# Kernel optimization log

Measured on AMD Instinct MI355X. Metric: run time of the kernel, lower is better.

## Reference

```python
import jax, jax.numpy as jnp
from jax import lax
import numpy as np

B, T, F = 64, 128, 16
H = 512
S = 2  # num_seg; SEG_DICT['2'] = [8, 6], seg_cumsum = [2, 10, 16]


def timestep_embedding(t, dim, max_period=10000.0):
    half = dim // 2
    freqs = jnp.exp(-jnp.log(max_period) * jnp.arange(half, dtype=jnp.float32) / half)
    args = t[:, None] * freqs  # [N, half]
    return jnp.concatenate([jnp.cos(args), jnp.sin(args)], axis=-1)  # [N, dim]


def setup_inputs() -> dict:
    key = jax.random.key(0)
    ks = jax.random.split(key, 16)
    sc = lambda *sh: 1.0 / np.sqrt(sh[-1])
    inp = {
        'x': jax.random.normal(ks[0], (B, T, F), dtype=jnp.float32),
        'lengths': jax.random.randint(ks[1], (B,), 1, T + 1),
        'h0': jax.random.uniform(ks[2], (B, H), dtype=jnp.float32),
        'c0': jax.random.uniform(ks[3], (B, H), dtype=jnp.float32),
        'W_is0': jax.random.normal(ks[4], (H, 8), dtype=jnp.float32) * sc(8),
        'b_is0': jax.random.normal(ks[5], (H,), dtype=jnp.float32) * 0.01,
        'W_is1': jax.random.normal(ks[6], (H, 6), dtype=jnp.float32) * sc(6),
        'b_is1': jax.random.normal(ks[7], (H,), dtype=jnp.float32) * 0.01,
        'W_ih': jax.random.normal(ks[8], (4 * H, 3 * H), dtype=jnp.float32) * sc(3 * H),
        'W_hh': jax.random.normal(ks[9], (4 * H, H), dtype=jnp.float32) * sc(H),
        'b_ih': jax.random.normal(ks[10], (4 * H,), dtype=jnp.float32) * 0.01,
        'b_hh': jax.random.normal(ks[11], (4 * H,), dtype=jnp.float32) * 0.01,
        'W_o': jax.random.normal(ks[12], (F - 2, S * H), dtype=jnp.float32) * sc(S * H),
        'b_o': jax.random.normal(ks[13], (F - 2,), dtype=jnp.float32) * 0.01,
    }
    return inp


def reference(x, lengths, h0, c0, W_is0, b_is0, W_is1, b_is1,
              W_ih, W_hh, b_ih, b_hh, W_o, b_o):
    b, t, f = x.shape
    h = h0.shape[1]
    xf = x.reshape(-1, f)  # [B*T, F]

    # timestep embeddings from the two time columns (learning_type='diff')
    tc = timestep_embedding(xf[:, 0], h)
    tp = timestep_embedding(xf[:, 1], h)
    t_emb = jnp.concatenate([tc, tp], axis=-1)  # [B*T, 2H]

    # per-segment input linears (segments = cols 2:10 and 10:16)
    e0 = xf[:, 2:10] @ W_is0.T + b_is0
    e1 = xf[:, 10:16] @ W_is1.T + b_is1
    e0 = jnp.concatenate([e0, t_emb], axis=-1)[:, None, :]  # [B*T, 1, 3H]
    e1 = jnp.concatenate([e1, t_emb], axis=-1)[:, None, :]
    # faithful to torch: concat on dim=1 then reshape(batch, num_seg, seq_len, -1)
    embs = jnp.concatenate([e0, e1], axis=1).reshape(b, S, t, 3 * h)

    def cell(carry, xt):
        hh, cc = carry
        gates = xt @ W_ih.T + b_ih + hh @ W_hh.T + b_hh
        i, fg, g, o = jnp.split(gates, 4, axis=-1)  # torch LSTMCell order i,f,g,o
        cc = jax.nn.sigmoid(fg) * cc + jax.nn.sigmoid(i) * jnp.tanh(g)
        hh = jax.nn.sigmoid(o) * jnp.tanh(cc)
        return (hh, cc), hh

    hs = []
    for s in range(S):  # shared cell weights across segments (same nn.LSTMCell object)
        xs = jnp.swapaxes(embs[:, s], 0, 1)  # [T, B, 3H]
        _, h_seq = lax.scan(cell, (h0, c0), xs)  # [T, B, H]
        hs.append(jnp.swapaxes(h_seq, 0, 1))  # [B, T, H]
    hidden_states = jnp.stack(hs, axis=-2)  # [B, T, S, H]; dropout rate 0 -> identity

    idx = lengths - 1  # final valid timestep per sequence
    hfin = hidden_states[jnp.arange(b), idx].reshape(b, S * h)  # [B, S*H]
    out = jax.nn.sigmoid(hfin @ W_o.T + b_o)  # mlp_o: Linear + Sigmoid
    return out
```

## Files before the change

kernel.cpp:

```cpp
#include <hip/hip_runtime.h>
#include <hip/hip_bf16.h>
#include <stdint.h>


typedef __attribute__((ext_vector_type(8))) short bf16x8_t;
typedef __attribute__((ext_vector_type(4))) float f32x4_t;

#define SENT 0xAAAAAAAAu

#define OFF_G      0u
#define OFF_TEMB   33554432u
#define OFF_HH     50331648u
#define OFF_WHH    67239936u
#define OFF_WMID   69337088u
#define OFF_WC0    73531392u
#define OFF_WC1    73596928u
#define OFF_BC     73662464u
#define OFF_HFIN   73678848u
#define OFF_GFLAG  73940992u

__device__ __forceinline__ float bf2f(uint16_t u){
  union { uint32_t i; float f; } v; v.i = ((uint32_t)u) << 16; return v.f;
}
__device__ __forceinline__ uint16_t f2b(float f){
  union { float f; uint32_t i; } v; v.f = f;
  uint32_t r = v.i + 0x7fffu + ((v.i >> 16) & 1u);
  return (uint16_t)(r >> 16);
}
__device__ __forceinline__ float sigm(float x){ return 1.0f/(1.0f + __expf(-x)); }
__device__ __forceinline__ float tanh_(float x){
  float xc = fminf(fmaxf(x, -15.f), 15.f);
  float t = __expf(2.f*xc);
  return (t - 1.f)/(t + 1.f);
}
__device__ __forceinline__ void gl_lds16(const void* g, void* l){
  __builtin_amdgcn_global_load_lds(
      (const __attribute__((address_space(1))) void*)g,
      (__attribute__((address_space(3))) void*)l, 16, 0, 0);
}

__global__ void prepAll(const float* __restrict__ x,
                        const float* __restrict__ W_ih, const float* __restrict__ W_hh,
                        const float* __restrict__ W_is0, const float* __restrict__ b_is0,
                        const float* __restrict__ W_is1, const float* __restrict__ b_is1,
                        const float* __restrict__ b_ih, const float* __restrict__ b_hh,
                        const float* __restrict__ h0,
                        uint16_t* __restrict__ whh_b, uint16_t* __restrict__ wmid_b,
                        float* __restrict__ wc0, float* __restrict__ wc1,
                        float* __restrict__ bc,
                        uint16_t* __restrict__ temb, uint16_t* __restrict__ h_hist,
                        uint32_t* __restrict__ gflag){
  const int bid = blockIdx.x, tid = threadIdx.x;
  if (bid < 2048){
    const int n = bid;
    __shared__ float wrow[512];
    __shared__ float red[16][17];
    wrow[tid]       = W_ih[(size_t)n*1536 + tid];
    wrow[tid + 256] = W_ih[(size_t)n*1536 + 256 + tid];
    for (int j = tid; j < 1024; j += 256)
      wmid_b[(size_t)n*1024 + j] = f2b(W_ih[(size_t)n*1536 + 512 + j]);
    for (int k = tid; k < 512; k += 256)
      whh_b[(size_t)n*512 + k] = f2b(W_hh[(size_t)n*512 + k]);
    __syncthreads();
    {
      const int d = tid >> 4, jp = tid & 15;
      float s = 0.f;
      const int kk0 = jp*32;
      if (d < 8){
        for (int k = kk0; k < kk0 + 32; ++k) s += wrow[k]*W_is0[k*8 + d];
      } else if (d < 14){
        int c = d - 8;
        for (int k = kk0; k < kk0 + 32; ++k) s += wrow[k]*W_is1[k*6 + c];
      } else if (d == 14){
        for (int k = kk0; k < kk0 + 32; ++k) s += wrow[k]*b_is0[k];
      } else {
        for (int k = kk0; k < kk0 + 32; ++k) s += wrow[k]*b_is1[k];
      }
      red[d][jp] = s;
    }
    __syncthreads();
    if (tid < 16){
      float tot = 0.f;
      #pragma unroll
      for (int i = 0; i < 16; ++i) tot += red[tid][i];
      if (tid < 8)        wc0[n*8 + tid] = tot;
      else if (tid < 14)  wc1[n*8 + (tid - 8)] = tot;
      else if (tid == 14) bc[n]        = b_ih[n] + b_hh[n] + tot;
      else                bc[2048 + n] = b_ih[n] + b_hh[n] + tot;
    } else if (tid == 16){
      wc1[n*8 + 6] = 0.f; wc1[n*8 + 7] = 0.f;
    }
  } else if (bid < 10240){
    const int rid = bid - 2048;
    const int k = tid;
    float x0 = x[(size_t)rid*16 + 0], x1 = x[(size_t)rid*16 + 1];
    float f = __expf((float)k * (-9.210340371976184f/256.f));
    float a0 = x0*f, a1 = x1*f;
    size_t base = (size_t)rid*1024;
    temb[base + k]        = f2b(__cosf(a0));
    temb[base + 256 + k]  = f2b(__sinf(a0));
    temb[base + 512 + k]  = f2b(__cosf(a1));
    temb[base + 768 + k]  = f2b(__sinf(a1));
  } else if (bid < 10368){
    int i = (bid - 10240)*256 + tid;
    uint32_t* hh = (uint32_t*)h_hist;
    int e    = i*2;
    int rrcg = e >> 9;
    int rr   = rrcg >> 4, cg = rrcg & 15;
    int rm   = e & 511;
    int row  = rm >> 5, u = rm & 31;
    int b    = (rr*16 + row) & 63;
    int unit = cg*32 + u;
    uint32_t lo = f2b(h0[(size_t)b*512 + unit]);
    uint32_t hi = f2b(h0[(size_t)b*512 + unit + 1]);
    uint32_t wd = lo | (hi << 16);
    if (wd == SENT) wd ^= 1u;
    hh[i] = wd;
    if (i < 1024) gflag[i] = 0u;
  } else {
    uint32_t* hh = (uint32_t*)h_hist;
    size_t w0 = 32768u + ((size_t)(bid - 10368)*256 + tid)*8;
    uint4 s4 = make_uint4(SENT, SENT, SENT, SENT);
    *(uint4*)&hh[w0]     = s4;
    *(uint4*)&hh[w0 + 4] = s4;
  }
}

__launch_bounds__(256)
__global__ void fusedk(const float* __restrict__ x, const float* __restrict__ c0,
                       const int* __restrict__ lengths,
                       const uint16_t* __restrict__ whh_b, const uint16_t* __restrict__ temb,
                       const uint16_t* __restrict__ wmid,
                       const float* __restrict__ wc0, const float* __restrict__ wc1,
                       const float* __restrict__ bc,
                       uint16_t* __restrict__ G, uint16_t* __restrict__ h_hist,
                       uint32_t* __restrict__ gflag, float* __restrict__ hfin){
  __shared__ __align__(16) uint16_t smem_u[17664];
  const int tid = threadIdx.x;
  const int bid = blockIdx.x;
  const int w = tid >> 6, lane = tid & 63;
  const int q = lane >> 4, ln = lane & 15;

  if (bid >= 128){
    const int gb = bid - 128;
    const int idx = gb >> 4;
    const int mt = (idx & 1) ? (idx >> 1) : (32 + (idx >> 1));
    const int n0 = (gb & 15)*128;
    uint16_t* Al = smem_u;
    uint16_t* Bl = smem_u + 8192;
    const int wm = w >> 1, wn = w & 1;
    const int srow_l = lane >> 3, scol = (lane & 7)*8;

    f32x4_t acc[4][4];
    #pragma unroll
    for (int a = 0; a < 4; ++a)
      #pragma unroll
      for (int b2 = 0; b2 < 4; ++b2) acc[a][b2] = (f32x4_t){0.f,0.f,0.f,0.f};

    for (int kb = 0; kb < 16; ++kb){
      #pragma unroll
      for (int i = 0; i < 4; ++i){
        int row0 = w*32 + i*8;
        int lrow = row0 + srow_l;
        int bA = lrow & 63, ntmA = mt*2 + (lrow >> 6);
        gl_lds16(temb + (size_t)(bA*128 + ntmA)*1024 + kb*64 + scol, &Al[row0*64]);
        gl_lds16(wmid + (size_t)(n0 + lrow)*1024 + kb*64 + scol, &Bl[row0*64]);
      }
      __syncthreads();
      #pragma unroll
      for (int kc = 0; kc < 2; ++kc){
        bf16x8_t af[4], bf[4];
        #pragma unroll
        for (int mt_i = 0; mt_i < 4; ++mt_i)
          af[mt_i] = *(const bf16x8_t*)&Al[(wm*64 + mt_i*16 + ln)*64 + kc*32 + q*8];
        #pragma unroll
        for (int nt = 0; nt < 4; ++nt)
          bf[nt] = *(const bf16x8_t*)&Bl[(wn*64 + nt*16 + ln)*64 + kc*32 + q*8];
        #pragma unroll
        for (int mt_i = 0; mt_i < 4; ++mt_i)
          #pragma unroll
          for (int nt = 0; nt < 4; ++nt)
            acc[mt_i][nt] = __builtin_amdgcn_mfma_f32_16x16x32_bf16(af[mt_i], bf[nt], acc[mt_i][nt], 0, 0, 0);
      }
      __syncthreads();
    }
    #pragma unroll
    for (int mt_i = 0; mt_i < 4; ++mt_i)
      #pragma unroll
      for (int nt = 0; nt < 4; ++nt)
        #pragma unroll
        for (int r = 0; r < 4; ++r){
          int Mr = wm*64 + mt_i*16 + q*4 + r;
          int Nc = wn*64 + nt*16 + ln;
          smem_u[Mr*128 + Nc] = f2b(acc[mt_i][nt][r]);
        }
    __syncthreads();
    {
      const int erow = tid >> 1, eh = tid & 1;
      const unsigned long long* lsrc = (const unsigned long long*)&smem_u[erow*128 + eh*64];
      unsigned long long* gdst = (unsigned long long*)
          (G + (size_t)(mt*128 + erow)*2048 + n0 + eh*64);
      #pragma unroll
      for (int i2 = 0; i2 < 16; ++i2)
        __hip_atomic_store(&gdst[i2], lsrc[i2], __ATOMIC_RELAXED, __HIP_MEMORY_SCOPE_AGENT);
    }
    __syncthreads();
    if (tid == 0)
      __hip_atomic_store(&gflag[mt*16 + (gb & 15)], 1u,
                         __ATOMIC_RELEASE, __HIP_MEMORY_SCOPE_AGENT);
    return;
  }

  #define HL(b,r,c) smem_u[(((b)*16 + (r))*552) + (c)]
  const int rr = bid & 7;
  const int g  = bid >> 3;
  const int k0 = g*32;
  const int sp = rr >> 2;
  const int u8 = ln & 7, gh = ln >> 3;
  const int unit = k0 + w*8 + u8;
  const int gl0 = gh*512 + unit;
  const int gl1 = (2 + gh)*512 + unit;
  const int LVL = 65536;

  bf16x8_t barr0[16], barr1[16];
  #pragma unroll
  for (int kc = 0; kc < 16; ++kc){
    barr0[kc] = *(const bf16x8_t*)(whh_b + (size_t)gl0*512 + kc*32 + q*8);
    barr1[kc] = *(const bf16x8_t*)(whh_b + (size_t)gl1*512 + kc*32 + q*8);
  }
  bf16x8_t e0f[2], e1f[2];
  #pragma unroll
  for (int nsI = 0; nsI < 2; ++nsI){
    bf16x8_t v0 = {0,0,0,0,0,0,0,0}, v1 = {0,0,0,0,0,0,0,0};
    if (q == 0){
      const float* wcs = nsI ? wc1 : wc0;
      #pragma unroll
      for (int jj = 0; jj < 8; ++jj){
        ((uint16_t*)&v0)[jj] = f2b(wcs[gl0*8 + jj]);
        ((uint16_t*)&v1)[jj] = f2b(wcs[gl1*8 + jj]);
      }
    }
    e0f[nsI] = v0; e1f[nsI] = v1;
  }
  float bc0v[2] = { bc[gl0], bc[2048 + gl0] };
  float bc1v[2] = { bc[gl1], bc[2048 + gl1] };

  int   bmr[4], lenr[4];
  float cst[4];
  #pragma unroll
  for (int r = 0; r < 4; ++r){
    int row = rr*16 + q*4 + r;
    bmr[r]  = row & 63;
    lenr[r] = lengths[bmr[r]];
    cst[r]  = c0[(size_t)bmr[r]*512 + unit];
  }

  const int prow = lane >> 2;
  const int pcol = (lane & 3)*8;
  const int xm = tid >> 3, xc = tid & 7;
  const int xb = (rr*16 + xm) & 63;
  const size_t stb = ((size_t)rr*8192 + g*512);

  for (int idx2 = tid; idx2 < 2*16*32; idx2 += 256)
    HL(idx2 >> 9, (idx2 >> 5) & 15, 520 + (idx2 & 31)) = 0;

  for (int t = 0; t < 128; ++t){
    const int qidx = sp*128 + t;
    const int ntm = qidx >> 1;
    const int ns  = qidx & 1;
    const int buf = t & 1;

    if ((t & 3) == 0){
      const int mt = qidx >> 2;
      const uint32_t* gf = gflag + mt*16 + (g >> 2);
      while (true){
        bool ok = true;
        #pragma unroll
        for (int j = 0; j < 4; ++j){
          uint32_t v = __hip_atomic_load(&gf[j*4], __ATOMIC_RELAXED, __HIP_MEMORY_SCOPE_AGENT);
          ok &= (v != 0u);
        }
        if (ok) break;
        __builtin_amdgcn_s_sleep(1);
      }
    }

    uint16_t g0r[4], g1r[4];
    #pragma unroll
    for (int r = 0; r < 4; ++r){
      size_t grow = (size_t)(ntm*64 + bmr[r])*2048;
      g0r[r] = G[grow + gl0];
      g1r[r] = G[grow + gl1];
    }
    float xv = 0.f;
    if (tid < 128){
      if (ns == 0)      xv = x[(size_t)(xb*128 + ntm)*16 + 2 + xc];
      else if (xc < 6)  xv = x[(size_t)(xb*128 + ntm)*16 + 10 + xc];
    }

    {
      const unsigned long long* lvl = (const unsigned long long*)h_hist
                                      + (((size_t)t*LVL + (size_t)rr*8192) >> 2);
      unsigned long long hv[4][2];
      while (true){
        bool ok = true;
        #pragma unroll
        for (int i = 0; i < 4; ++i){
          const unsigned long long* p = lvl + ((size_t)(w*4 + i)*128 + prow*8 + (pcol >> 2));
          hv[i][0] = __hip_atomic_load(&p[0], __ATOMIC_RELAXED, __HIP_MEMORY_SCOPE_AGENT);
          hv[i][1] = __hip_atomic_load(&p[1], __ATOMIC_RELAXED, __HIP_MEMORY_SCOPE_AGENT);
          ok &= ((uint32_t)hv[i][0] != SENT) & ((uint32_t)(hv[i][0] >> 32) != SENT)
              & ((uint32_t)hv[i][1] != SENT) & ((uint32_t)(hv[i][1] >> 32) != SENT);
        }
        if (__all(ok)) break;
        __builtin_amdgcn_s_sleep(1);
      }
      #pragma unroll
      for (int i = 0; i < 4; ++i){
        int reg = w*4 + i;
        *(unsigned long long*)&HL(buf, prow, reg*32 + pcol)     = hv[i][0];
        *(unsigned long long*)&HL(buf, prow, reg*32 + pcol + 4) = hv[i][1];
      }
    }
    if (tid < 128) HL(buf, xm, 512 + xc) = f2b(xv);
    __syncthreads();

    f32x4_t acc0, acc1;
    {
      float b0 = ns ? bc0v[1] : bc0v[0];
      float b1 = ns ? bc1v[1] : bc1v[0];
      #pragma unroll
      for (int r = 0; r < 4; ++r){ acc0[r] = bf2f(g0r[r]) + b0; acc1[r] = bf2f(g1r[r]) + b1; }
    }
    #pragma unroll
    for (int kc = 0; kc < 16; ++kc){
      bf16x8_t a = *(const bf16x8_t*)&HL(buf, ln, kc*32 + q*8);
      acc0 = __builtin_amdgcn_mfma_f32_16x16x32_bf16(a, barr0[kc], acc0, 0, 0, 0);
      acc1 = __builtin_amdgcn_mfma_f32_16x16x32_bf16(a, barr1[kc], acc1, 0, 0, 0);
    }
    {
      bf16x8_t a = *(const bf16x8_t*)&HL(buf, ln, 512 + q*8);
      acc0 = __builtin_amdgcn_mfma_f32_16x16x32_bf16(a, ns ? e0f[1] : e0f[0], acc0, 0, 0, 0);
      acc1 = __builtin_amdgcn_mfma_f32_16x16x32_bf16(a, ns ? e1f[1] : e1f[0], acc1, 0, 0, 0);
    }

    float pf[4], po[4];
    #pragma unroll
    for (int r = 0; r < 4; ++r){
      pf[r] = __shfl_xor(acc0[r], 8);
      po[r] = __shfl_xor(acc1[r], 8);
    }
    if (ln < 8){
      uint32_t hb[4]; float hF[4];
      #pragma unroll
      for (int r = 0; r < 4; ++r){
        float ig = acc0[r], fg = pf[r], gg = acc1[r], og = po[r];
        cst[r] = sigm(fg)*cst[r] + sigm(ig)*tanh_(gg);
        float h = sigm(og)*tanh_(cst[r]);
        hF[r] = h; hb[r] = (uint32_t)f2b(h);
      }
      #pragma unroll
      for (int r = 0; r < 4; ++r){
        uint32_t ph = (uint32_t)__shfl_xor((int)hb[r], 1);
        uint32_t packed = hb[r] | (ph << 16);
        if (packed == SENT) packed ^= 1u;
        uint32_t hi = (uint32_t)__shfl_xor((int)packed, 2);
        if ((ln & 3) == 0){
          unsigned long long v = (unsigned long long)packed | ((unsigned long long)hi << 32);
          unsigned long long* hp = (unsigned long long*)h_hist
              + (((size_t)(t+1)*LVL + stb + (size_t)(q*4 + r)*32 + w*8 + u8) >> 2);
          __hip_atomic_store(hp, v, __ATOMIC_RELAXED, __HIP_MEMORY_SCOPE_AGENT);
        }
        if (t == lenr[r] - 1)
          hfin[(size_t)bmr[r]*1024 + sp*512 + unit] = hF[r];
      }
    }
  }
  #undef HL
}

__global__ void outk(const float* __restrict__ hfin, const float* __restrict__ W_o,
                     const float* __restrict__ b_o, float* __restrict__ out){
  __shared__ float hl[1024];
  __shared__ float red[16][17];
  const int b = blockIdx.x, tid = threadIdx.x;
  #pragma unroll
  for (int i = 0; i < 4; ++i) hl[tid + i*256] = hfin[(size_t)b*1024 + tid + i*256];
  __syncthreads();
  const int o = tid >> 4, j0 = tid & 15;
  float s = 0.f;
  if (o < 14){
    for (int j = j0; j < 1024; j += 16) s += hl[j]*W_o[(size_t)o*1024 + j];
  }
  red[o][j0] = s;
  __syncthreads();
  if (tid < 14){
    float tot = b_o[tid];
    #pragma unroll
    for (int i = 0; i < 16; ++i) tot += red[tid][i];
    out[b*14 + tid] = 1.0f/(1.0f + __expf(-tot));
  }
}

extern "C" void kernel_launch(void* const* d_in, const int* in_sizes, int n_in,
                              void* d_out, int out_size, void* d_ws, size_t ws_size,
                              hipStream_t stream){
  const float* x     = (const float*)d_in[0];
  const int*   lens  = (const int*)  d_in[1];
  const float* h0    = (const float*)d_in[2];
  const float* c0    = (const float*)d_in[3];
  const float* W_is0 = (const float*)d_in[4];
  const float* b_is0 = (const float*)d_in[5];
  const float* W_is1 = (const float*)d_in[6];
  const float* b_is1 = (const float*)d_in[7];
  const float* W_ih  = (const float*)d_in[8];
  const float* W_hh  = (const float*)d_in[9];
  const float* b_ih  = (const float*)d_in[10];
  const float* b_hh  = (const float*)d_in[11];
  const float* W_o   = (const float*)d_in[12];
  const float* b_o   = (const float*)d_in[13];
  float* out = (float*)d_out;

  char* ws = (char*)d_ws;
  uint16_t* G      = (uint16_t*)(ws + OFF_G);
  uint16_t* temb   = (uint16_t*)(ws + OFF_TEMB);
  uint16_t* h_hist = (uint16_t*)(ws + OFF_HH);
  uint16_t* whh_b  = (uint16_t*)(ws + OFF_WHH);
  uint16_t* wmid_b = (uint16_t*)(ws + OFF_WMID);
  float* wc0  = (float*)(ws + OFF_WC0);
  float* wc1  = (float*)(ws + OFF_WC1);
  float* bc   = (float*)(ws + OFF_BC);
  float* hfin = (float*)(ws + OFF_HFIN);
  uint32_t* gflag = (uint32_t*)(ws + OFF_GFLAG);

  hipLaunchKernelGGL(prepAll, dim3(12416), dim3(256), 0, stream,
                     x, W_ih, W_hh, W_is0, b_is0, W_is1, b_is1, b_ih, b_hh, h0,
                     whh_b, wmid_b, wc0, wc1, bc, temb, h_hist, gflag);
  hipLaunchKernelGGL(fusedk, dim3(1152), dim3(256), 0, stream,
                     x, c0, lens, whh_b, temb, wmid_b, wc0, wc1, bc,
                     G, h_hist, gflag, hfin);
  hipLaunchKernelGGL(outk, dim3(64), dim3(256), 0, stream, hfin, W_o, b_o, out);
}
```

Before: 569.1 us.

## Compute timestep embeddings inside the GEMM tile loader instead of materializing them

Removes the prep-kernel pass that wrote a 16 MB bf16 timestep-embedding buffer. The input-projection GEMM blocks now compute cos and sin of x*freq on the fly and write them directly into LDS, rather than loading them from global memory. This cuts global traffic and prep-kernel blocks at the cost of recomputing transcendentals per k-block in the GEMM. It also raises wave priority for the recurrent blocks via s_setprio so they are favoured over the GEMM producer blocks.

```diff
diff --git a/kernel.cpp b/kernel.cpp
--- a/kernel.cpp
+++ b/kernel.cpp
@@ -9,7 +9,6 @@
 #define SENT 0xAAAAAAAAu
 
 #define OFF_G      0u
-#define OFF_TEMB   33554432u
 #define OFF_HH     50331648u
 #define OFF_WHH    67239936u
 #define OFF_WMID   69337088u
@@ -39,8 +38,7 @@
       (__attribute__((address_space(3))) void*)l, 16, 0, 0);
 }
 
-__global__ void prepAll(const float* __restrict__ x,
-                        const float* __restrict__ W_ih, const float* __restrict__ W_hh,
+__global__ void prepAll(const float* __restrict__ W_ih, const float* __restrict__ W_hh,
                         const float* __restrict__ W_is0, const float* __restrict__ b_is0,
                         const float* __restrict__ W_is1, const float* __restrict__ b_is1,
                         const float* __restrict__ b_ih, const float* __restrict__ b_hh,
@@ -48,8 +46,7 @@
                         uint16_t* __restrict__ whh_b, uint16_t* __restrict__ wmid_b,
                         float* __restrict__ wc0, float* __restrict__ wc1,
                         float* __restrict__ bc,
-                        uint16_t* __restrict__ temb, uint16_t* __restrict__ h_hist,
-                        uint32_t* __restrict__ gflag){
+                        uint16_t* __restrict__ h_hist, uint32_t* __restrict__ gflag){
   const int bid = blockIdx.x, tid = threadIdx.x;
   if (bid < 2048){
     const int n = bid;
@@ -90,19 +87,8 @@
     } else if (tid == 16){
       wc1[n*8 + 6] = 0.f; wc1[n*8 + 7] = 0.f;
     }
-  } else if (bid < 10240){
-    const int rid = bid - 2048;
-    const int k = tid;
-    float x0 = x[(size_t)rid*16 + 0], x1 = x[(size_t)rid*16 + 1];
-    float f = __expf((float)k * (-9.210340371976184f/256.f));
-    float a0 = x0*f, a1 = x1*f;
-    size_t base = (size_t)rid*1024;
-    temb[base + k]        = f2b(__cosf(a0));
-    temb[base + 256 + k]  = f2b(__sinf(a0));
-    temb[base + 512 + k]  = f2b(__cosf(a1));
-    temb[base + 768 + k]  = f2b(__sinf(a1));
-  } else if (bid < 10368){
-    int i = (bid - 10240)*256 + tid;
+  } else if (bid < 2176){
+    int i = (bid - 2048)*256 + tid;
     uint32_t* hh = (uint32_t*)h_hist;
     int e    = i*2;
     int rrcg = e >> 9;
@@ -119,7 +105,7 @@
     if (i < 1024) gflag[i] = 0u;
   } else {
     uint32_t* hh = (uint32_t*)h_hist;
-    size_t w0 = 32768u + ((size_t)(bid - 10368)*256 + tid)*8;
+    size_t w0 = 32768u + ((size_t)(bid - 2176)*256 + tid)*8;
     uint4 s4 = make_uint4(SENT, SENT, SENT, SENT);
     *(uint4*)&hh[w0]     = s4;
     *(uint4*)&hh[w0 + 4] = s4;
@@ -129,8 +115,7 @@
 __launch_bounds__(256)
 __global__ void fusedk(const float* __restrict__ x, const float* __restrict__ c0,
                        const int* __restrict__ lengths,
-                       const uint16_t* __restrict__ whh_b, const uint16_t* __restrict__ temb,
-                       const uint16_t* __restrict__ wmid,
+                       const uint16_t* __restrict__ whh_b, const uint16_t* __restrict__ wmid,
                        const float* __restrict__ wc0, const float* __restrict__ wc1,
                        const float* __restrict__ bc,
                        uint16_t* __restrict__ G, uint16_t* __restrict__ h_hist,
@@ -151,6 +136,15 @@
     const int wm = w >> 1, wn = w & 1;
     const int srow_l = lane >> 3, scol = (lane & 7)*8;
 
+    float xs[4][2];
+    #pragma unroll
+    for (int i = 0; i < 4; ++i){
+      int lrow = w*32 + i*8 + srow_l;
+      int bA = lrow & 63, ntmA = mt*2 + (lrow >> 6);
+      xs[i][0] = x[(size_t)(bA*128 + ntmA)*16 + 0];
+      xs[i][1] = x[(size_t)(bA*128 + ntmA)*16 + 1];
+    }
+
     f32x4_t acc[4][4];
     #pragma unroll
     for (int a = 0; a < 4; ++a)
@@ -161,10 +155,27 @@
       #pragma unroll
       for (int i = 0; i < 4; ++i){
         int row0 = w*32 + i*8;
-        int lrow = row0 + srow_l;
-        int bA = lrow & 63, ntmA = mt*2 + (lrow >> 6);
-        gl_lds16(temb + (size_t)(bA*128 + ntmA)*1024 + kb*64 + scol, &Al[row0*64]);
-        gl_lds16(wmid + (size_t)(n0 + lrow)*1024 + kb*64 + scol, &Bl[row0*64]);
+        gl_lds16(wmid + (size_t)(n0 + row0 + srow_l)*1024 + kb*64 + scol, &Bl[row0*64]);
+      }
+      {
+        uint16_t av[4][8];
+        #pragma unroll
+        for (int j = 0; j < 8; ++j){
+          int col = kb*64 + scol + j;
+          int sel = col >> 8;
+          float f = __expf((float)(col & 255) * (-9.210340371976184f/256.f));
+          #pragma unroll
+          for (int i = 0; i < 4; ++i){
+            float a = xs[i][sel >> 1]*f;
+            float v = (sel & 1) ? __sinf(a) : __cosf(a);
+            av[i][j] = f2b(v);
+          }
+        }
+        #pragma unroll
+        for (int i = 0; i < 4; ++i){
+          int lrow = w*32 + i*8 + srow_l;
+          *(uint4*)&Al[lrow*64 + scol] = *(uint4*)av[i];
+        }
       }
       __syncthreads();
       #pragma unroll
@@ -211,6 +222,7 @@
     return;
   }
 
+  asm volatile("s_setprio 3");
   #define HL(b,r,c) smem_u[(((b)*16 + (r))*552) + (c)]
   const int rr = bid & 7;
   const int g  = bid >> 3;
@@ -423,7 +435,6 @@
 
   char* ws = (char*)d_ws;
   uint16_t* G      = (uint16_t*)(ws + OFF_G);
-  uint16_t* temb   = (uint16_t*)(ws + OFF_TEMB);
   uint16_t* h_hist = (uint16_t*)(ws + OFF_HH);
   uint16_t* whh_b  = (uint16_t*)(ws + OFF_WHH);
   uint16_t* wmid_b = (uint16_t*)(ws + OFF_WMID);
@@ -433,11 +444,11 @@
   float* hfin = (float*)(ws + OFF_HFIN);
   uint32_t* gflag = (uint32_t*)(ws + OFF_GFLAG);
 
-  hipLaunchKernelGGL(prepAll, dim3(12416), dim3(256), 0, stream,
-                     x, W_ih, W_hh, W_is0, b_is0, W_is1, b_is1, b_ih, b_hh, h0,
-                     whh_b, wmid_b, wc0, wc1, bc, temb, h_hist, gflag);
+  hipLaunchKernelGGL(prepAll, dim3(4224), dim3(256), 0, stream,
+                     W_ih, W_hh, W_is0, b_is0, W_is1, b_is1, b_ih, b_hh, h0,
+                     whh_b, wmid_b, wc0, wc1, bc, h_hist, gflag);
   hipLaunchKernelGGL(fusedk, dim3(1152), dim3(256), 0, stream,
-                     x, c0, lens, whh_b, temb, wmid_b, wc0, wc1, bc,
+                     x, c0, lens, whh_b, wmid_b, wc0, wc1, bc,
                      G, h_hist, gflag, hfin);
   hipLaunchKernelGGL(outk, dim3(64), dim3(256), 0, stream, hfin, W_o, b_o, out);
 }
```

Measured after the change: 571.6 us. About the same (+0.4%).
